# Kernel tuning notes

Hardware: AMD Instinct MI355X
Metric: run time of the kernel (lower is better)

## Reference

```python
import jax, jax.numpy as jnp
import numpy as np

D_MODEL = 1024
D_K = 1024
D_V = 1024
THRESH = 0.9
LN_EPS = 1e-6


def setup_inputs() -> dict:
    key = jax.random.key(0)
    ks = jax.random.split(key, 8)
    B, S = 8, 2048
    scale = 1.0 / np.sqrt(D_MODEL)
    return {
        "q": jax.random.normal(ks[0], (B, S, D_MODEL), dtype=jnp.float32),
        "k": jax.random.normal(ks[1], (B, S, D_MODEL), dtype=jnp.float32),
        "v": jax.random.normal(ks[2], (B, S, D_MODEL), dtype=jnp.float32),
        "Wq": jax.random.normal(ks[3], (D_MODEL, D_K), dtype=jnp.float32) * scale,
        "Wk": jax.random.normal(ks[4], (D_MODEL, D_K), dtype=jnp.float32) * scale,
        "Wv": jax.random.normal(ks[5], (D_MODEL, D_V), dtype=jnp.float32) * scale,
        "Wfc": jax.random.normal(ks[6], (D_V, D_MODEL), dtype=jnp.float32) * (1.0 / np.sqrt(D_V)),
        "ln_gamma": jnp.ones((D_MODEL,), dtype=jnp.float32),
        "ln_beta": jnp.zeros((D_MODEL,), dtype=jnp.float32),
    }


def reference(q, k, v, Wq, Wk, Wv, Wfc, ln_gamma, ln_beta):
    residual = q
    qh = q @ Wq          # [B,S,d_k]
    kh = k @ Wk          # [B,S,d_k]
    vh = v @ Wv          # [B,S,d_v]
    inv_sqrt_dk = jnp.asarray(1.0 / np.sqrt(D_K), dtype=qh.dtype)
    attn = jnp.einsum('bqd,bkd->bqk', qh, kh) * inv_sqrt_dk  # [B,S,S]
    # hard sparsity threshold applied BEFORE softmax (faithful to original)
    attn = jnp.where(attn < THRESH, jnp.asarray(0.0, attn.dtype), attn)
    attn = jax.nn.softmax(attn, axis=-1)
    # dropout is identity in eval mode
    out = jnp.einsum('bqk,bkd->bqd', attn, vh) @ Wfc  # [B,S,d_model]
    out = out + residual
    mean = jnp.mean(out, axis=-1, keepdims=True)
    var = jnp.mean(jnp.square(out - mean), axis=-1, keepdims=True)
    out = (out - mean) * jax.lax.rsqrt(var + LN_EPS) * ln_gamma + ln_beta
    return (out, attn)
```

## Files before the change

kernel.cpp:

```cpp
#include <hip/hip_runtime.h>
#include <hip/hip_bf16.h>
#include <stdint.h>

typedef __attribute__((ext_vector_type(8))) short bf16x8;
typedef __attribute__((ext_vector_type(4))) float f32x4;
typedef __attribute__((ext_vector_type(4))) unsigned short us4;
typedef __attribute__((ext_vector_type(8))) unsigned short us8;

__device__ __forceinline__ unsigned short f2bf(float f) {
  union { float f; unsigned int u; } v; v.f = f;
  unsigned int u = v.u;
  return (unsigned short)((u + 0x7FFFu + ((u >> 16) & 1u)) >> 16);
}
__device__ __forceinline__ float bf2f(unsigned short h) {
  union { unsigned int u; float f; } v; v.u = ((unsigned int)h) << 16;
  return v.f;
}

__device__ __forceinline__ void gload16(const unsigned short* g, unsigned short* l) {
  __builtin_amdgcn_global_load_lds(
      (const __attribute__((address_space(1))) unsigned int*)g,
      (__attribute__((address_space(3))) unsigned int*)l, 16, 0, 0);
}

template <int EPI>
__global__ __launch_bounds__(256, 2)
void gemm_nt(const unsigned short* __restrict__ Ap, const unsigned short* __restrict__ Btp,
             void* __restrict__ Cp, float* __restrict__ extra,
             int M, int N, int K, int nbm,
             long long sA, long long sB, long long sC)
{
  const int tid = threadIdx.x;
  const int lane = tid & 63;
  const int wid = tid >> 6;
  const int wr = wid >> 1, wc = wid & 1;
  const int bb = blockIdx.y;
  const int bm = blockIdx.x % nbm, bn = blockIdx.x / nbm;
  const int row0 = bm * 128, col0 = bn * 128;

  __shared__ unsigned short lsA[128 * 64];
  __shared__ unsigned short lsB[128 * 64];
  __shared__ float srow2[128][2];

  const unsigned short* Ab = Ap + (long long)bb * sA;
  const unsigned short* Bb = Btp + (long long)bb * sB;

  const int srow = wid * 32 + (lane >> 3);
  const int sslot = (lane & 7) ^ (lane >> 3);
  const unsigned short* Asrc = Ab + (long long)(row0 + srow) * K + sslot * 8;
  const unsigned short* Bsrc = Bb + (long long)(col0 + srow) * K + sslot * 8;
  unsigned short* ldsA0 = &lsA[wid * 2048];
  unsigned short* ldsB0 = &lsB[wid * 2048];

  f32x4 acc[4][4];
#pragma unroll
  for (int i = 0; i < 4; ++i)
#pragma unroll
    for (int j = 0; j < 4; ++j) {
      f32x4 z = {0.f, 0.f, 0.f, 0.f};
      acc[i][j] = z;
    }

  for (int k0 = 0; k0 < K; k0 += 64) {
    __syncthreads();
#pragma unroll
    for (int it = 0; it < 4; ++it) {
      gload16(Asrc + (long long)it * 8 * K + k0, ldsA0 + it * 512);
      gload16(Bsrc + (long long)it * 8 * K + k0, ldsB0 + it * 512);
    }
    __syncthreads();
#pragma unroll
    for (int kk = 0; kk < 2; ++kk) {
      int kslot = kk * 4 + (lane >> 4);
      bf16x8 af[4], bfg[4];
#pragma unroll
      for (int mf = 0; mf < 4; ++mf) {
        int rl = wr * 64 + mf * 16 + (lane & 15);
        af[mf] = *(const bf16x8*)&lsA[rl * 64 + ((kslot ^ (rl & 7)) * 8)];
      }
#pragma unroll
      for (int nf = 0; nf < 4; ++nf) {
        int cl = wc * 64 + nf * 16 + (lane & 15);
        bfg[nf] = *(const bf16x8*)&lsB[cl * 64 + ((kslot ^ (cl & 7)) * 8)];
      }
#pragma unroll
      for (int mf = 0; mf < 4; ++mf)
#pragma unroll
        for (int nf = 0; nf < 4; ++nf)
          acc[mf][nf] = __builtin_amdgcn_mfma_f32_16x16x32_bf16(af[mf], bfg[nf], acc[mf][nf], 0, 0, 0);
    }
  }

  if (EPI == 0) {
    unsigned short* C = (unsigned short*)Cp + (long long)bb * sC;
#pragma unroll
    for (int mf = 0; mf < 4; ++mf)
#pragma unroll
      for (int nf = 0; nf < 4; ++nf)
#pragma unroll
        for (int i = 0; i < 4; ++i) {
          int gr = row0 + wr * 64 + mf * 16 + (lane >> 4) * 4 + i;
          int gc = col0 + wc * 64 + nf * 16 + (lane & 15);
          C[(long long)gr * N + gc] = f2bf(acc[mf][nf][i]);
        }
  } else if (EPI == 2) {
    unsigned short* C = (unsigned short*)Cp;
#pragma unroll
    for (int mf = 0; mf < 4; ++mf)
#pragma unroll
      for (int nf = 0; nf < 4; ++nf) {
        int gr = row0 + wr * 64 + mf * 16 + (lane >> 4) * 4;
        int gc = col0 + wc * 64 + nf * 16 + (lane & 15);
        int bb2 = gr >> 11, grb = gr & 2047;
        us4 o;
        o[0] = f2bf(acc[mf][nf][0]); o[1] = f2bf(acc[mf][nf][1]);
        o[2] = f2bf(acc[mf][nf][2]); o[3] = f2bf(acc[mf][nf][3]);
        *(us4*)&C[(long long)bb2 * sC + (long long)gc * 2048 + grb] = o;
      }
  } else if (EPI == 3) {
    unsigned short* C = (unsigned short*)Cp + (long long)bb * sC;
    const float* inv = extra + (long long)bb * 2048;
#pragma unroll
    for (int mf = 0; mf < 4; ++mf)
#pragma unroll
      for (int nf = 0; nf < 4; ++nf)
#pragma unroll
        for (int i = 0; i < 4; ++i) {
          int gr = row0 + wr * 64 + mf * 16 + (lane >> 4) * 4 + i;
          int gc = col0 + wc * 64 + nf * 16 + (lane & 15);
          C[(long long)gr * N + gc] = f2bf(acc[mf][nf][i] * inv[gr]);
        }
  } else {
    unsigned short* C = (unsigned short*)Cp + (long long)bb * sC;
    float rs[4][4];
#pragma unroll
    for (int mf = 0; mf < 4; ++mf)
#pragma unroll
      for (int i = 0; i < 4; ++i) rs[mf][i] = 0.f;
#pragma unroll
    for (int mf = 0; mf < 4; ++mf)
#pragma unroll
      for (int nf = 0; nf < 4; ++nf)
#pragma unroll
        for (int i = 0; i < 4; ++i) {
          int gr = row0 + wr * 64 + mf * 16 + (lane >> 4) * 4 + i;
          int gc = col0 + wc * 64 + nf * 16 + (lane & 15);
          float s = acc[mf][nf][i] * 0.03125f;
          s = (s < 0.9f) ? 0.f : s;
          float e = __expf(s);
          C[(long long)gr * N + gc] = f2bf(e);
          rs[mf][i] += e;
        }
#pragma unroll
    for (int mf = 0; mf < 4; ++mf)
#pragma unroll
      for (int i = 0; i < 4; ++i) {
        float vv = rs[mf][i];
        vv += __shfl_xor(vv, 1); vv += __shfl_xor(vv, 2);
        vv += __shfl_xor(vv, 4); vv += __shfl_xor(vv, 8);
        if ((lane & 15) == 0)
          srow2[wr * 64 + mf * 16 + (lane >> 4) * 4 + i][wc] = vv;
      }
    __syncthreads();
    if (tid < 128) {
      int gr = row0 + tid;
      extra[((long long)bb * M + gr) * 16 + bn] = srow2[tid][0] + srow2[tid][1];
    }
  }
}

__global__ __launch_bounds__(256)
void cvt3(const float* __restrict__ a, const float* __restrict__ b,
          const float* __restrict__ c, unsigned short* __restrict__ oa,
          unsigned short* __restrict__ ob, unsigned short* __restrict__ oc) {
  const long long i = ((long long)blockIdx.x * 256 + threadIdx.x) * 8;
#pragma unroll
  for (int p = 0; p < 3; ++p) {
    const float* src = (p == 0) ? a : (p == 1) ? b : c;
    unsigned short* dst = (p == 0) ? oa : (p == 1) ? ob : oc;
    f32x4 x0 = *(const f32x4*)(src + i);
    f32x4 x1 = *(const f32x4*)(src + i + 4);
    us8 o;
    o[0] = f2bf(x0[0]); o[1] = f2bf(x0[1]); o[2] = f2bf(x0[2]); o[3] = f2bf(x0[3]);
    o[4] = f2bf(x1[0]); o[5] = f2bf(x1[1]); o[6] = f2bf(x1[2]); o[7] = f2bf(x1[3]);
    *(us8*)(dst + i) = o;
  }
}

__global__ __launch_bounds__(256)
void wtrans(const float* __restrict__ W, unsigned short* __restrict__ WT) {
  __shared__ float t[32][33];
  const int bi = blockIdx.x, bj = blockIdx.y;
  const int c = threadIdx.x & 31;
  const int r0 = threadIdx.x >> 5;
#pragma unroll
  for (int j = 0; j < 4; ++j) {
    int r = r0 + j * 8;
    t[r][c] = W[(long long)(bi * 32 + r) * 1024 + bj * 32 + c];
  }
  __syncthreads();
#pragma unroll
  for (int j = 0; j < 4; ++j) {
    int r = r0 + j * 8;
    WT[(long long)(bj * 32 + r) * 1024 + bi * 32 + c] = f2bf(t[c][r]);
  }
}

__global__ __launch_bounds__(256)
void attn_norm(const unsigned short* __restrict__ e, const float* __restrict__ partials,
               float* __restrict__ attn, float* __restrict__ inv_dens) {
  const long long row = blockIdx.x;
  const int tid = threadIdx.x;
  __shared__ float sden;
  if (tid < 64) {
    float v = (tid < 16) ? partials[row * 16 + tid] : 0.f;
    v += __shfl_xor(v, 1); v += __shfl_xor(v, 2);
    v += __shfl_xor(v, 4); v += __shfl_xor(v, 8);
    if (tid == 0) sden = v;
  }
  __syncthreads();
  const float inv = 1.0f / sden;
  if (tid == 0) inv_dens[row] = inv;
  us8 x = *(const us8*)(e + row * 2048 + tid * 8);
  f32x4 y0, y1;
#pragma unroll
  for (int i = 0; i < 4; ++i) { y0[i] = bf2f(x[i]) * inv; y1[i] = bf2f(x[i + 4]) * inv; }
  *(f32x4*)(attn + row * 2048 + tid * 8) = y0;
  *(f32x4*)(attn + row * 2048 + tid * 8 + 4) = y1;
}

__global__ __launch_bounds__(256)
void ln_kernel(const unsigned short* __restrict__ fc, const float* __restrict__ q,
               const float* __restrict__ gamma, const float* __restrict__ beta,
               float* __restrict__ out) {
  const long long row = blockIdx.x;
  const int tid = threadIdx.x;
  __shared__ float sb1[4], sb2[4];
  us4 hv = *(const us4*)(fc + row * 1024 + tid * 4);
  f32x4 qv = *(const f32x4*)(q + row * 1024 + tid * 4);
  float x0 = bf2f(hv[0]) + qv[0];
  float x1 = bf2f(hv[1]) + qv[1];
  float x2 = bf2f(hv[2]) + qv[2];
  float x3 = bf2f(hv[3]) + qv[3];
  float s = x0 + x1 + x2 + x3;
#pragma unroll
  for (int m = 1; m < 64; m <<= 1) s += __shfl_xor(s, m);
  if ((tid & 63) == 0) sb1[tid >> 6] = s;
  __syncthreads();
  const float mean = (sb1[0] + sb1[1] + sb1[2] + sb1[3]) * (1.0f / 1024.0f);
  float d0 = x0 - mean, d1 = x1 - mean, d2 = x2 - mean, d3 = x3 - mean;
  float vs = d0 * d0 + d1 * d1 + d2 * d2 + d3 * d3;
#pragma unroll
  for (int m = 1; m < 64; m <<= 1) vs += __shfl_xor(vs, m);
  if ((tid & 63) == 0) sb2[tid >> 6] = vs;
  __syncthreads();
  const float var = (sb2[0] + sb2[1] + sb2[2] + sb2[3]) * (1.0f / 1024.0f);
  const float r = rsqrtf(var + 1e-6f);
  f32x4 g = *(const f32x4*)(gamma + tid * 4);
  f32x4 bt = *(const f32x4*)(beta + tid * 4);
  f32x4 o;
  o[0] = d0 * r * g[0] + bt[0];
  o[1] = d1 * r * g[1] + bt[1];
  o[2] = d2 * r * g[2] + bt[2];
  o[3] = d3 * r * g[3] + bt[3];
  *(f32x4*)(out + row * 1024 + tid * 4) = o;
}

extern "C" void kernel_launch(void* const* d_in, const int* in_sizes, int n_in,
                              void* d_out, int out_size, void* d_ws, size_t ws_size,
                              hipStream_t stream) {
  const float* q    = (const float*)d_in[0];
  const float* k    = (const float*)d_in[1];
  const float* v    = (const float*)d_in[2];
  const float* Wq   = (const float*)d_in[3];
  const float* Wk   = (const float*)d_in[4];
  const float* Wv   = (const float*)d_in[5];
  const float* Wfc  = (const float*)d_in[6];
  const float* gamma = (const float*)d_in[7];
  const float* beta  = (const float*)d_in[8];

  float* out0 = (float*)d_out;
  float* attn = out0 + (long long)8 * 2048 * 1024;

  char* ao = (char*)attn;
  unsigned short* qb = (unsigned short*)(ao);
  unsigned short* kb = (unsigned short*)(ao + (32ll << 20));
  unsigned short* vb = (unsigned short*)(ao + (64ll << 20));
  unsigned short* qh = (unsigned short*)(ao + (96ll << 20));
  unsigned short* kh = (unsigned short*)(ao);
  unsigned short* vhT     = (unsigned short*)d_out;
  unsigned short* out_mid = (unsigned short*)((char*)d_out + (32ll << 20));

  char* ws = (char*)d_ws;
  unsigned short* WqT  = (unsigned short*)(ws);
  unsigned short* WkT  = (unsigned short*)(ws + (2ll  << 20));
  unsigned short* WvT  = (unsigned short*)(ws + (4ll  << 20));
  unsigned short* WfcT = (unsigned short*)(ws + (6ll  << 20));
  float* partials      = (float*)(ws + (8ll  << 20));
  float* inv_dens      = (float*)(ws + (10ll << 20));
  unsigned short* e    = (unsigned short*)(ws + (11ll << 20));
  unsigned short* fc   = e;

  cvt3<<<dim3(8192), 256, 0, stream>>>(q, k, v, qb, kb, vb);
  wtrans<<<dim3(32, 32), 256, 0, stream>>>(Wq, WqT);
  wtrans<<<dim3(32, 32), 256, 0, stream>>>(Wk, WkT);
  wtrans<<<dim3(32, 32), 256, 0, stream>>>(Wv, WvT);
  wtrans<<<dim3(32, 32), 256, 0, stream>>>(Wfc, WfcT);

  gemm_nt<0><<<dim3(1024, 1), 256, 0, stream>>>(qb, WqT, qh, nullptr,
      16384, 1024, 1024, 128, 0, 0, 0);
  gemm_nt<0><<<dim3(1024, 1), 256, 0, stream>>>(kb, WkT, kh, nullptr,
      16384, 1024, 1024, 128, 0, 0, 0);
  gemm_nt<2><<<dim3(1024, 1), 256, 0, stream>>>(vb, WvT, vhT, nullptr,
      16384, 1024, 1024, 128, 0, 0, 1024ll * 2048);

  gemm_nt<1><<<dim3(256, 8), 256, 0, stream>>>(qh, kh, e, partials,
      2048, 2048, 1024, 16, 2048ll * 1024, 2048ll * 1024, 2048ll * 2048);

  attn_norm<<<dim3(16384), 256, 0, stream>>>(e, partials, attn, inv_dens);

  gemm_nt<3><<<dim3(128, 8), 256, 0, stream>>>(e, vhT, out_mid, inv_dens,
      2048, 1024, 2048, 16, 2048ll * 2048, 1024ll * 2048, 2048ll * 1024);

  gemm_nt<0><<<dim3(1024, 1), 256, 0, stream>>>(out_mid, WfcT, fc, nullptr,
      16384, 1024, 1024, 128, 0, 0, 0);

  ln_kernel<<<dim3(16384), 256, 0, stream>>>(fc, q, gamma, beta, out0);
}
```

Measured before the change: 420.5 us.

## Replace 128x128 GEMM with 256x256 8-wave double-buffered pipelined GEMM

Swaps the 128x128-tile, 4-wave single-buffered GEMM for a 256x256-tile, 8-wave kernel. It double-buffers LDS, prefetches the next K-tile in quarter phases guarded by vmcnt waits, and raises wave priority around the MFMA bursts. The goal is to hide global-load latency behind compute and raise operand reuse per LDS byte. The row-sum partials shrink to 8 per row, so attn_norm changes to match. The cost is 128 KB of LDS per block and fewer blocks, which can leave CUs idle on the smaller batched GEMMs.

Measured after the change: 445.7 us. 6.0% more time.

```diff
diff --git a/kernel.cpp b/kernel.cpp
--- a/kernel.cpp
+++ b/kernel.cpp
@@ -24,149 +24,201 @@
 }
 
 template <int EPI>
-__global__ __launch_bounds__(256, 2)
-void gemm_nt(const unsigned short* __restrict__ Ap, const unsigned short* __restrict__ Btp,
-             void* __restrict__ Cp, float* __restrict__ extra,
-             int M, int N, int K, int nbm,
-             long long sA, long long sB, long long sC)
+__global__ __launch_bounds__(512, 2)
+void gemm8(const unsigned short* __restrict__ Ap, const unsigned short* __restrict__ Btp,
+           void* __restrict__ Cp, float* __restrict__ extra,
+           int M, int N, int K, int nbm, int nbn,
+           long long sA, long long sB, long long sC)
 {
+  __shared__ unsigned short ls[65536];
+  __shared__ float srow[256][4];
+
   const int tid = threadIdx.x;
   const int lane = tid & 63;
   const int wid = tid >> 6;
-  const int wr = wid >> 1, wc = wid & 1;
   const int bb = blockIdx.y;
   const int bm = blockIdx.x % nbm, bn = blockIdx.x / nbm;
-  const int row0 = bm * 128, col0 = bn * 128;
-
-  __shared__ unsigned short lsA[128 * 64];
-  __shared__ unsigned short lsB[128 * 64];
-  __shared__ float srow2[128][2];
+  const int row0 = bm * 256, col0 = bn * 256;
 
   const unsigned short* Ab = Ap + (long long)bb * sA;
   const unsigned short* Bb = Btp + (long long)bb * sB;
 
-  const int srow = wid * 32 + (lane >> 3);
-  const int sslot = (lane & 7) ^ (lane >> 3);
-  const unsigned short* Asrc = Ab + (long long)(row0 + srow) * K + sslot * 8;
-  const unsigned short* Bsrc = Bb + (long long)(col0 + srow) * K + sslot * 8;
-  unsigned short* ldsA0 = &lsA[wid * 2048];
-  unsigned short* ldsB0 = &lsB[wid * 2048];
-
-  f32x4 acc[4][4];
-#pragma unroll
-  for (int i = 0; i < 4; ++i)
-#pragma unroll
-    for (int j = 0; j < 4; ++j) {
-      f32x4 z = {0.f, 0.f, 0.f, 0.f};
-      acc[i][j] = z;
-    }
-
-  for (int k0 = 0; k0 < K; k0 += 64) {
-    __syncthreads();
-#pragma unroll
-    for (int it = 0; it < 4; ++it) {
-      gload16(Asrc + (long long)it * 8 * K + k0, ldsA0 + it * 512);
-      gload16(Bsrc + (long long)it * 8 * K + k0, ldsB0 + it * 512);
-    }
-    __syncthreads();
-#pragma unroll
-    for (int kk = 0; kk < 2; ++kk) {
-      int kslot = kk * 4 + (lane >> 4);
-      bf16x8 af[4], bfg[4];
-#pragma unroll
-      for (int mf = 0; mf < 4; ++mf) {
-        int rl = wr * 64 + mf * 16 + (lane & 15);
-        af[mf] = *(const bf16x8*)&lsA[rl * 64 + ((kslot ^ (rl & 7)) * 8)];
-      }
-#pragma unroll
-      for (int nf = 0; nf < 4; ++nf) {
-        int cl = wc * 64 + nf * 16 + (lane & 15);
-        bfg[nf] = *(const bf16x8*)&lsB[cl * 64 + ((kslot ^ (cl & 7)) * 8)];
-      }
-#pragma unroll
-      for (int mf = 0; mf < 4; ++mf)
-#pragma unroll
-        for (int nf = 0; nf < 4; ++nf)
-          acc[mf][nf] = __builtin_amdgcn_mfma_f32_16x16x32_bf16(af[mf], bfg[nf], acc[mf][nf], 0, 0, 0);
-    }
-  }
-
-  if (EPI == 0) {
+  const int sr = tid >> 3;
+  const int sslot = (tid & 7) ^ (sr & 7);
+  const unsigned short* Asrc = Ab + (long long)(row0 + sr) * K + sslot * 8;
+  const unsigned short* Bsrc = Bb + (long long)(col0 + sr) * K + sslot * 8;
+  unsigned short* lsw = ls + wid * 512;
+
+#define ISSUE_A(HALF, BUFOFF, KOFF) do { \
+    gload16(Asrc + (long long)((HALF) * 128) * K + (KOFF), lsw + (BUFOFF) + (HALF) * 8192); \
+    gload16(Asrc + (long long)((HALF) * 128 + 64) * K + (KOFF), lsw + (BUFOFF) + (HALF) * 8192 + 4096); \
+  } while (0)
+#define ISSUE_B(HALF, BUFOFF, KOFF) do { \
+    gload16(Bsrc + (long long)((HALF) * 128) * K + (KOFF), lsw + (BUFOFF) + (2 + (HALF)) * 8192); \
+    gload16(Bsrc + (long long)((HALF) * 128 + 64) * K + (KOFF), lsw + (BUFOFF) + (2 + (HALF)) * 8192 + 4096); \
+  } while (0)
+
+  const int warow = ((wid >> 2) * 64) + (lane & 15);
+  const int wbcol = ((wid & 3) * 32) + (lane & 15);
+
+  f32x4 acc[2][2][4][2];
+#pragma unroll
+  for (int a = 0; a < 2; ++a)
+#pragma unroll
+    for (int b = 0; b < 2; ++b)
+#pragma unroll
+      for (int m = 0; m < 4; ++m)
+#pragma unroll
+        for (int n = 0; n < 2; ++n) {
+          f32x4 z = {0.f, 0.f, 0.f, 0.f};
+          acc[a][b][m][n] = z;
+        }
+
+#define PHASE(HA, HB) do { \
+    const unsigned short* Ah = ls + cur + (HA) * 8192; \
+    const unsigned short* Bh = ls + cur + (2 + (HB)) * 8192; \
+    _Pragma("unroll") \
+    for (int kk = 0; kk < 2; ++kk) { \
+      const int kslot = kk * 4 + (lane >> 4); \
+      bf16x8 af[4], bfr[2]; \
+      _Pragma("unroll") \
+      for (int mf = 0; mf < 4; ++mf) { \
+        const int rl = warow + mf * 16; \
+        af[mf] = *(const bf16x8*)&Ah[rl * 64 + ((kslot ^ (rl & 7)) * 8)]; \
+      } \
+      _Pragma("unroll") \
+      for (int nf = 0; nf < 2; ++nf) { \
+        const int cl = wbcol + nf * 16; \
+        bfr[nf] = *(const bf16x8*)&Bh[cl * 64 + ((kslot ^ (cl & 7)) * 8)]; \
+      } \
+      __builtin_amdgcn_s_setprio(1); \
+      _Pragma("unroll") \
+      for (int mf = 0; mf < 4; ++mf) \
+        _Pragma("unroll") \
+        for (int nf = 0; nf < 2; ++nf) \
+          acc[HA][HB][mf][nf] = __builtin_amdgcn_mfma_f32_16x16x32_bf16( \
+              af[mf], bfr[nf], acc[HA][HB][mf][nf], 0, 0, 0); \
+      __builtin_amdgcn_s_setprio(0); \
+    } \
+  } while (0)
+
+#define WAITBAR() do { \
+    asm volatile("s_waitcnt vmcnt(4)" ::: "memory"); \
+    __builtin_amdgcn_s_barrier(); \
+    __builtin_amdgcn_sched_barrier(0); \
+  } while (0)
+
+  ISSUE_A(0, 0, 0);
+  ISSUE_B(0, 0, 0);
+  ISSUE_A(1, 0, 0);
+  ISSUE_B(1, 0, 0);
+
+  const int NT = K >> 6;
+  for (int t = 0; t < NT; ++t) {
+    const int cur = (t & 1) << 15;
+    const int nxt = ((t + 1) & 1) << 15;
+    const long long ko = (long long)(t + 1) * 64;
+    const bool pf = (t + 1 < NT);
+    WAITBAR();
+    if (pf) ISSUE_A(0, nxt, ko);
+    PHASE(0, 0);
+    WAITBAR();
+    if (pf) ISSUE_B(0, nxt, ko);
+    PHASE(1, 0);
+    WAITBAR();
+    if (pf) ISSUE_A(1, nxt, ko);
+    PHASE(0, 1);
+    if (pf) ISSUE_B(1, nxt, ko);
+    PHASE(1, 1);
+  }
+
+  if (EPI == 0 || EPI == 3) {
     unsigned short* C = (unsigned short*)Cp + (long long)bb * sC;
-#pragma unroll
-    for (int mf = 0; mf < 4; ++mf)
-#pragma unroll
-      for (int nf = 0; nf < 4; ++nf)
-#pragma unroll
-        for (int i = 0; i < 4; ++i) {
-          int gr = row0 + wr * 64 + mf * 16 + (lane >> 4) * 4 + i;
-          int gc = col0 + wc * 64 + nf * 16 + (lane & 15);
-          C[(long long)gr * N + gc] = f2bf(acc[mf][nf][i]);
-        }
+    const float* inv = (EPI == 3) ? (extra + (long long)bb * 2048) : nullptr;
+#pragma unroll
+    for (int ha = 0; ha < 2; ++ha)
+#pragma unroll
+      for (int hb = 0; hb < 2; ++hb)
+#pragma unroll
+        for (int mf = 0; mf < 4; ++mf)
+#pragma unroll
+          for (int nf = 0; nf < 2; ++nf)
+#pragma unroll
+            for (int i = 0; i < 4; ++i) {
+              int gr = row0 + ha * 128 + (wid >> 2) * 64 + mf * 16 + (lane >> 4) * 4 + i;
+              int gc = col0 + hb * 128 + (wid & 3) * 32 + nf * 16 + (lane & 15);
+              float x = acc[ha][hb][mf][nf][i];
+              if (EPI == 3) x *= inv[gr];
+              C[(long long)gr * N + gc] = f2bf(x);
+            }
   } else if (EPI == 2) {
     unsigned short* C = (unsigned short*)Cp;
 #pragma unroll
-    for (int mf = 0; mf < 4; ++mf)
-#pragma unroll
-      for (int nf = 0; nf < 4; ++nf) {
-        int gr = row0 + wr * 64 + mf * 16 + (lane >> 4) * 4;
-        int gc = col0 + wc * 64 + nf * 16 + (lane & 15);
-        int bb2 = gr >> 11, grb = gr & 2047;
-        us4 o;
-        o[0] = f2bf(acc[mf][nf][0]); o[1] = f2bf(acc[mf][nf][1]);
-        o[2] = f2bf(acc[mf][nf][2]); o[3] = f2bf(acc[mf][nf][3]);
-        *(us4*)&C[(long long)bb2 * sC + (long long)gc * 2048 + grb] = o;
-      }
-  } else if (EPI == 3) {
-    unsigned short* C = (unsigned short*)Cp + (long long)bb * sC;
-    const float* inv = extra + (long long)bb * 2048;
-#pragma unroll
-    for (int mf = 0; mf < 4; ++mf)
-#pragma unroll
-      for (int nf = 0; nf < 4; ++nf)
-#pragma unroll
-        for (int i = 0; i < 4; ++i) {
-          int gr = row0 + wr * 64 + mf * 16 + (lane >> 4) * 4 + i;
-          int gc = col0 + wc * 64 + nf * 16 + (lane & 15);
-          C[(long long)gr * N + gc] = f2bf(acc[mf][nf][i] * inv[gr]);
-        }
+    for (int ha = 0; ha < 2; ++ha)
+#pragma unroll
+      for (int hb = 0; hb < 2; ++hb)
+#pragma unroll
+        for (int mf = 0; mf < 4; ++mf)
+#pragma unroll
+          for (int nf = 0; nf < 2; ++nf) {
+            int gr = row0 + ha * 128 + (wid >> 2) * 64 + mf * 16 + (lane >> 4) * 4;
+            int gc = col0 + hb * 128 + (wid & 3) * 32 + nf * 16 + (lane & 15);
+            int bb2 = gr >> 11, grb = gr & 2047;
+            us4 o;
+            o[0] = f2bf(acc[ha][hb][mf][nf][0]); o[1] = f2bf(acc[ha][hb][mf][nf][1]);
+            o[2] = f2bf(acc[ha][hb][mf][nf][2]); o[3] = f2bf(acc[ha][hb][mf][nf][3]);
+            *(us4*)&C[(long long)bb2 * sC + (long long)gc * 2048 + grb] = o;
+          }
   } else {
     unsigned short* C = (unsigned short*)Cp + (long long)bb * sC;
-    float rs[4][4];
-#pragma unroll
-    for (int mf = 0; mf < 4; ++mf)
-#pragma unroll
-      for (int i = 0; i < 4; ++i) rs[mf][i] = 0.f;
-#pragma unroll
-    for (int mf = 0; mf < 4; ++mf)
-#pragma unroll
-      for (int nf = 0; nf < 4; ++nf)
+    float rs[2][4][4];
+#pragma unroll
+    for (int ha = 0; ha < 2; ++ha)
+#pragma unroll
+      for (int mf = 0; mf < 4; ++mf)
+#pragma unroll
+        for (int i = 0; i < 4; ++i) rs[ha][mf][i] = 0.f;
+#pragma unroll
+    for (int ha = 0; ha < 2; ++ha)
+#pragma unroll
+      for (int hb = 0; hb < 2; ++hb)
+#pragma unroll
+        for (int mf = 0; mf < 4; ++mf)
+#pragma unroll
+          for (int nf = 0; nf < 2; ++nf)
+#pragma unroll
+            for (int i = 0; i < 4; ++i) {
+              int gr = row0 + ha * 128 + (wid >> 2) * 64 + mf * 16 + (lane >> 4) * 4 + i;
+              int gc = col0 + hb * 128 + (wid & 3) * 32 + nf * 16 + (lane & 15);
+              float s = acc[ha][hb][mf][nf][i] * 0.03125f;
+              s = (s < 0.9f) ? 0.f : s;
+              float e = __expf(s);
+              C[(long long)gr * N + gc] = f2bf(e);
+              rs[ha][mf][i] += e;
+            }
+#pragma unroll
+    for (int ha = 0; ha < 2; ++ha)
+#pragma unroll
+      for (int mf = 0; mf < 4; ++mf)
 #pragma unroll
         for (int i = 0; i < 4; ++i) {
-          int gr = row0 + wr * 64 + mf * 16 + (lane >> 4) * 4 + i;
-          int gc = col0 + wc * 64 + nf * 16 + (lane & 15);
-          float s = acc[mf][nf][i] * 0.03125f;
-          s = (s < 0.9f) ? 0.f : s;
-          float e = __expf(s);
-          C[(long long)gr * N + gc] = f2bf(e);
-          rs[mf][i] += e;
+          float vv = rs[ha][mf][i];
+          vv += __shfl_xor(vv, 1); vv += __shfl_xor(vv, 2);
+          vv += __shfl_xor(vv, 4); vv += __shfl_xor(vv, 8);
+          if ((lane & 15) == 0)
+            srow[ha * 128 + (wid >> 2) * 64 + mf * 16 + (lane >> 4) * 4 + i][wid & 3] = vv;
         }
-#pragma unroll
-    for (int mf = 0; mf < 4; ++mf)
-#pragma unroll
-      for (int i = 0; i < 4; ++i) {
-        float vv = rs[mf][i];
-        vv += __shfl_xor(vv, 1); vv += __shfl_xor(vv, 2);
-        vv += __shfl_xor(vv, 4); vv += __shfl_xor(vv, 8);
-        if ((lane & 15) == 0)
-          srow2[wr * 64 + mf * 16 + (lane >> 4) * 4 + i][wc] = vv;
-      }
     __syncthreads();
-    if (tid < 128) {
+    if (tid < 256) {
       int gr = row0 + tid;
-      extra[((long long)bb * M + gr) * 16 + bn] = srow2[tid][0] + srow2[tid][1];
+      extra[((long long)bb * M + gr) * nbn + bn] =
+          srow[tid][0] + srow[tid][1] + srow[tid][2] + srow[tid][3];
     }
   }
+#undef PHASE
+#undef WAITBAR
+#undef ISSUE_A
+#undef ISSUE_B
 }
 
 __global__ __launch_bounds__(256)
@@ -213,9 +265,8 @@
   const int tid = threadIdx.x;
   __shared__ float sden;
   if (tid < 64) {
-    float v = (tid < 16) ? partials[row * 16 + tid] : 0.f;
-    v += __shfl_xor(v, 1); v += __shfl_xor(v, 2);
-    v += __shfl_xor(v, 4); v += __shfl_xor(v, 8);
+    float v = (tid < 8) ? partials[row * 8 + tid] : 0.f;
+    v += __shfl_xor(v, 1); v += __shfl_xor(v, 2); v += __shfl_xor(v, 4);
     if (tid == 0) sden = v;
   }
   __syncthreads();
@@ -307,23 +358,23 @@
   wtrans<<<dim3(32, 32), 256, 0, stream>>>(Wv, WvT);
   wtrans<<<dim3(32, 32), 256, 0, stream>>>(Wfc, WfcT);
 
-  gemm_nt<0><<<dim3(1024, 1), 256, 0, stream>>>(qb, WqT, qh, nullptr,
-      16384, 1024, 1024, 128, 0, 0, 0);
-  gemm_nt<0><<<dim3(1024, 1), 256, 0, stream>>>(kb, WkT, kh, nullptr,
-      16384, 1024, 1024, 128, 0, 0, 0);
-  gemm_nt<2><<<dim3(1024, 1), 256, 0, stream>>>(vb, WvT, vhT, nullptr,
-      16384, 1024, 1024, 128, 0, 0, 1024ll * 2048);
-
-  gemm_nt<1><<<dim3(256, 8), 256, 0, stream>>>(qh, kh, e, partials,
-      2048, 2048, 1024, 16, 2048ll * 1024, 2048ll * 1024, 2048ll * 2048);
+  gemm8<0><<<dim3(256, 1), 512, 0, stream>>>(qb, WqT, qh, nullptr,
+      16384, 1024, 1024, 64, 4, 0, 0, 0);
+  gemm8<0><<<dim3(256, 1), 512, 0, stream>>>(kb, WkT, kh, nullptr,
+      16384, 1024, 1024, 64, 4, 0, 0, 0);
+  gemm8<2><<<dim3(256, 1), 512, 0, stream>>>(vb, WvT, vhT, nullptr,
+      16384, 1024, 1024, 64, 4, 0, 0, 1024ll * 2048);
+
+  gemm8<1><<<dim3(64, 8), 512, 0, stream>>>(qh, kh, e, partials,
+      2048, 2048, 1024, 8, 8, 2048ll * 1024, 2048ll * 1024, 2048ll * 2048);
 
   attn_norm<<<dim3(16384), 256, 0, stream>>>(e, partials, attn, inv_dens);
 
-  gemm_nt<3><<<dim3(128, 8), 256, 0, stream>>>(e, vhT, out_mid, inv_dens,
-      2048, 1024, 2048, 16, 2048ll * 2048, 1024ll * 2048, 2048ll * 1024);
-
-  gemm_nt<0><<<dim3(1024, 1), 256, 0, stream>>>(out_mid, WfcT, fc, nullptr,
-      16384, 1024, 1024, 128, 0, 0, 0);
+  gemm8<3><<<dim3(32, 8), 512, 0, stream>>>(e, vhT, out_mid, inv_dens,
+      2048, 1024, 2048, 8, 4, 2048ll * 2048, 1024ll * 2048, 2048ll * 1024);
+
+  gemm8<0><<<dim3(256, 1), 512, 0, stream>>>(out_mid, WfcT, fc, nullptr,
+      16384, 1024, 1024, 64, 4, 0, 0, 0);
 
   ln_kernel<<<dim3(16384), 256, 0, stream>>>(fc, q, gamma, beta, out0);
 }
```

## Replace GEMM with 256x256-tile triple-buffered pipelined kernel using 8 waves

Applied to the files above, without the earlier changes.

Replaces the 128x128, 256-thread GEMM with a 256x256-tile, 512-thread kernel that keeps three BK=32 LDS buffers and prefetches two K-steps ahead, using explicit vmcnt waits and a single barrier per step. It also raises MFMA priority around the compute block and reduces per-tile row-sum partials from 16 to 8, updating attn_norm to match. The aim is to overlap global loads with MFMA and raise arithmetic intensity per LDS byte. In exchange, register pressure is much higher (8x4 accumulators), occupancy drops to one block per CU, and the grids shrink to 256 blocks, which may underfill the 256 CUs for some launches.

New measurement: 446.2 us. 1.06x slower.

```diff
diff --git a/kernel.cpp b/kernel.cpp
--- a/kernel.cpp
+++ b/kernel.cpp
@@ -24,127 +24,131 @@
 }
 
 template <int EPI>
-__global__ __launch_bounds__(256, 2)
-void gemm_nt(const unsigned short* __restrict__ Ap, const unsigned short* __restrict__ Btp,
-             void* __restrict__ Cp, float* __restrict__ extra,
-             int M, int N, int K, int nbm,
-             long long sA, long long sB, long long sC)
+__global__ __launch_bounds__(512, 1)
+void gemm9(const unsigned short* __restrict__ Ap, const unsigned short* __restrict__ Btp,
+           void* __restrict__ Cp, float* __restrict__ extra,
+           int M, int N, int K, int nbm, int nbn,
+           long long sA, long long sB, long long sC)
 {
+  __shared__ unsigned short ls[3 * 16384];
+  __shared__ float srow[256][4];
+
   const int tid = threadIdx.x;
   const int lane = tid & 63;
   const int wid = tid >> 6;
-  const int wr = wid >> 1, wc = wid & 1;
   const int bb = blockIdx.y;
   const int bm = blockIdx.x % nbm, bn = blockIdx.x / nbm;
-  const int row0 = bm * 128, col0 = bn * 128;
-
-  __shared__ unsigned short lsA[128 * 64];
-  __shared__ unsigned short lsB[128 * 64];
-  __shared__ float srow2[128][2];
+  const int row0 = bm * 256, col0 = bn * 256;
 
   const unsigned short* Ab = Ap + (long long)bb * sA;
   const unsigned short* Bb = Btp + (long long)bb * sB;
 
-  const int srow = wid * 32 + (lane >> 3);
-  const int sslot = (lane & 7) ^ (lane >> 3);
-  const unsigned short* Asrc = Ab + (long long)(row0 + srow) * K + sslot * 8;
-  const unsigned short* Bsrc = Bb + (long long)(col0 + srow) * K + sslot * 8;
-  unsigned short* ldsA0 = &lsA[wid * 2048];
-  unsigned short* ldsB0 = &lsB[wid * 2048];
-
-  f32x4 acc[4][4];
-#pragma unroll
-  for (int i = 0; i < 4; ++i)
-#pragma unroll
-    for (int j = 0; j < 4; ++j) {
+  const int stgrow = wid * 32 + (lane >> 2);
+  const int sslot = (lane & 3) ^ ((lane >> 2) & 3);
+  const unsigned short* Asrc = Ab + (long long)(row0 + stgrow) * K + sslot * 8;
+  const unsigned short* Bsrc = Bb + (long long)(col0 + stgrow) * K + sslot * 8;
+
+  const int warow = (wid >> 2) * 128 + (lane & 15);
+  const int wbcol = (wid & 3) * 64 + (lane & 15);
+  const int rslot = ((lane >> 4) ^ (lane & 3)) * 8;
+
+#define ISSUE(KT, CB) do { \
+    unsigned short* _la = ls + (CB) * 16384 + wid * 1024; \
+    unsigned short* _lb = _la + 8192; \
+    const long long _ko = (long long)(KT) * 32; \
+    gload16(Asrc + _ko, _la); \
+    gload16(Asrc + 16ll * K + _ko, _la + 512); \
+    gload16(Bsrc + _ko, _lb); \
+    gload16(Bsrc + 16ll * K + _ko, _lb + 512); \
+  } while (0)
+
+  f32x4 acc[8][4];
+#pragma unroll
+  for (int m = 0; m < 8; ++m)
+#pragma unroll
+    for (int n = 0; n < 4; ++n) {
       f32x4 z = {0.f, 0.f, 0.f, 0.f};
-      acc[i][j] = z;
+      acc[m][n] = z;
     }
 
-  for (int k0 = 0; k0 < K; k0 += 64) {
-    __syncthreads();
-#pragma unroll
-    for (int it = 0; it < 4; ++it) {
-      gload16(Asrc + (long long)it * 8 * K + k0, ldsA0 + it * 512);
-      gload16(Bsrc + (long long)it * 8 * K + k0, ldsB0 + it * 512);
+  const int NT = K >> 5;
+  ISSUE(0, 0);
+  ISSUE(1, 1);
+
+  int c0 = 0, c1 = 1, c2 = 2;
+  for (int t = 0; t < NT; ++t) {
+    if (t + 1 < NT) asm volatile("s_waitcnt vmcnt(4)" ::: "memory");
+    else            asm volatile("s_waitcnt vmcnt(0)" ::: "memory");
+    __builtin_amdgcn_s_barrier();
+    __builtin_amdgcn_sched_barrier(0);
+    if (t + 2 < NT) ISSUE(t + 2, c2);
+    {
+      const unsigned short* _A = ls + c0 * 16384;
+      const unsigned short* _B = _A + 8192;
+      bf16x8 af[8], bfr[4];
+#pragma unroll
+      for (int mf = 0; mf < 8; ++mf)
+        af[mf] = *(const bf16x8*)&_A[(warow + mf * 16) * 32 + rslot];
+#pragma unroll
+      for (int nf = 0; nf < 4; ++nf)
+        bfr[nf] = *(const bf16x8*)&_B[(wbcol + nf * 16) * 32 + rslot];
+      __builtin_amdgcn_s_setprio(1);
+#pragma unroll
+      for (int mf = 0; mf < 8; ++mf)
+#pragma unroll
+        for (int nf = 0; nf < 4; ++nf)
+          acc[mf][nf] = __builtin_amdgcn_mfma_f32_16x16x32_bf16(
+              af[mf], bfr[nf], acc[mf][nf], 0, 0, 0);
+      __builtin_amdgcn_s_setprio(0);
     }
-    __syncthreads();
-#pragma unroll
-    for (int kk = 0; kk < 2; ++kk) {
-      int kslot = kk * 4 + (lane >> 4);
-      bf16x8 af[4], bfg[4];
-#pragma unroll
-      for (int mf = 0; mf < 4; ++mf) {
-        int rl = wr * 64 + mf * 16 + (lane & 15);
-        af[mf] = *(const bf16x8*)&lsA[rl * 64 + ((kslot ^ (rl & 7)) * 8)];
-      }
-#pragma unroll
-      for (int nf = 0; nf < 4; ++nf) {
-        int cl = wc * 64 + nf * 16 + (lane & 15);
-        bfg[nf] = *(const bf16x8*)&lsB[cl * 64 + ((kslot ^ (cl & 7)) * 8)];
-      }
-#pragma unroll
-      for (int mf = 0; mf < 4; ++mf)
-#pragma unroll
-        for (int nf = 0; nf < 4; ++nf)
-          acc[mf][nf] = __builtin_amdgcn_mfma_f32_16x16x32_bf16(af[mf], bfg[nf], acc[mf][nf], 0, 0, 0);
-    }
-  }
-
-  if (EPI == 0) {
+    int tmp = c0; c0 = c1; c1 = c2; c2 = tmp;
+  }
+#undef ISSUE
+
+  if (EPI == 0 || EPI == 3) {
     unsigned short* C = (unsigned short*)Cp + (long long)bb * sC;
-#pragma unroll
-    for (int mf = 0; mf < 4; ++mf)
+    const float* inv = (EPI == 3) ? (extra + (long long)bb * 2048) : nullptr;
+#pragma unroll
+    for (int mf = 0; mf < 8; ++mf)
 #pragma unroll
       for (int nf = 0; nf < 4; ++nf)
 #pragma unroll
         for (int i = 0; i < 4; ++i) {
-          int gr = row0 + wr * 64 + mf * 16 + (lane >> 4) * 4 + i;
-          int gc = col0 + wc * 64 + nf * 16 + (lane & 15);
-          C[(long long)gr * N + gc] = f2bf(acc[mf][nf][i]);
+          int gr = row0 + (wid >> 2) * 128 + mf * 16 + (lane >> 4) * 4 + i;
+          int gc = col0 + (wid & 3) * 64 + nf * 16 + (lane & 15);
+          float x = acc[mf][nf][i];
+          if (EPI == 3) x *= inv[gr];
+          C[(long long)gr * N + gc] = f2bf(x);
         }
   } else if (EPI == 2) {
     unsigned short* C = (unsigned short*)Cp;
 #pragma unroll
-    for (int mf = 0; mf < 4; ++mf)
+    for (int mf = 0; mf < 8; ++mf)
 #pragma unroll
       for (int nf = 0; nf < 4; ++nf) {
-        int gr = row0 + wr * 64 + mf * 16 + (lane >> 4) * 4;
-        int gc = col0 + wc * 64 + nf * 16 + (lane & 15);
+        int gr = row0 + (wid >> 2) * 128 + mf * 16 + (lane >> 4) * 4;
+        int gc = col0 + (wid & 3) * 64 + nf * 16 + (lane & 15);
         int bb2 = gr >> 11, grb = gr & 2047;
         us4 o;
         o[0] = f2bf(acc[mf][nf][0]); o[1] = f2bf(acc[mf][nf][1]);
         o[2] = f2bf(acc[mf][nf][2]); o[3] = f2bf(acc[mf][nf][3]);
         *(us4*)&C[(long long)bb2 * sC + (long long)gc * 2048 + grb] = o;
       }
-  } else if (EPI == 3) {
-    unsigned short* C = (unsigned short*)Cp + (long long)bb * sC;
-    const float* inv = extra + (long long)bb * 2048;
-#pragma unroll
-    for (int mf = 0; mf < 4; ++mf)
-#pragma unroll
-      for (int nf = 0; nf < 4; ++nf)
-#pragma unroll
-        for (int i = 0; i < 4; ++i) {
-          int gr = row0 + wr * 64 + mf * 16 + (lane >> 4) * 4 + i;
-          int gc = col0 + wc * 64 + nf * 16 + (lane & 15);
-          C[(long long)gr * N + gc] = f2bf(acc[mf][nf][i] * inv[gr]);
-        }
   } else {
     unsigned short* C = (unsigned short*)Cp + (long long)bb * sC;
-    float rs[4][4];
-#pragma unroll
-    for (int mf = 0; mf < 4; ++mf)
+    float rs[8][4];
+#pragma unroll
+    for (int mf = 0; mf < 8; ++mf)
 #pragma unroll
       for (int i = 0; i < 4; ++i) rs[mf][i] = 0.f;
 #pragma unroll
-    for (int mf = 0; mf < 4; ++mf)
+    for (int mf = 0; mf < 8; ++mf)
 #pragma unroll
       for (int nf = 0; nf < 4; ++nf)
 #pragma unroll
         for (int i = 0; i < 4; ++i) {
-          int gr = row0 + wr * 64 + mf * 16 + (lane >> 4) * 4 + i;
-          int gc = col0 + wc * 64 + nf * 16 + (lane & 15);
+          int gr = row0 + (wid >> 2) * 128 + mf * 16 + (lane >> 4) * 4 + i;
+          int gc = col0 + (wid & 3) * 64 + nf * 16 + (lane & 15);
           float s = acc[mf][nf][i] * 0.03125f;
           s = (s < 0.9f) ? 0.f : s;
           float e = __expf(s);
@@ -152,19 +156,20 @@
           rs[mf][i] += e;
         }
 #pragma unroll
-    for (int mf = 0; mf < 4; ++mf)
+    for (int mf = 0; mf < 8; ++mf)
 #pragma unroll
       for (int i = 0; i < 4; ++i) {
         float vv = rs[mf][i];
         vv += __shfl_xor(vv, 1); vv += __shfl_xor(vv, 2);
         vv += __shfl_xor(vv, 4); vv += __shfl_xor(vv, 8);
         if ((lane & 15) == 0)
-          srow2[wr * 64 + mf * 16 + (lane >> 4) * 4 + i][wc] = vv;
+          srow[(wid >> 2) * 128 + mf * 16 + (lane >> 4) * 4 + i][wid & 3] = vv;
       }
     __syncthreads();
-    if (tid < 128) {
+    if (tid < 256) {
       int gr = row0 + tid;
-      extra[((long long)bb * M + gr) * 16 + bn] = srow2[tid][0] + srow2[tid][1];
+      extra[((long long)bb * M + gr) * nbn + bn] =
+          srow[tid][0] + srow[tid][1] + srow[tid][2] + srow[tid][3];
     }
   }
 }
@@ -213,9 +218,8 @@
   const int tid = threadIdx.x;
   __shared__ float sden;
   if (tid < 64) {
-    float v = (tid < 16) ? partials[row * 16 + tid] : 0.f;
-    v += __shfl_xor(v, 1); v += __shfl_xor(v, 2);
-    v += __shfl_xor(v, 4); v += __shfl_xor(v, 8);
+    float v = (tid < 8) ? partials[row * 8 + tid] : 0.f;
+    v += __shfl_xor(v, 1); v += __shfl_xor(v, 2); v += __shfl_xor(v, 4);
     if (tid == 0) sden = v;
   }
   __syncthreads();
@@ -307,23 +311,23 @@
   wtrans<<<dim3(32, 32), 256, 0, stream>>>(Wv, WvT);
   wtrans<<<dim3(32, 32), 256, 0, stream>>>(Wfc, WfcT);
 
-  gemm_nt<0><<<dim3(1024, 1), 256, 0, stream>>>(qb, WqT, qh, nullptr,
-      16384, 1024, 1024, 128, 0, 0, 0);
-  gemm_nt<0><<<dim3(1024, 1), 256, 0, stream>>>(kb, WkT, kh, nullptr,
-      16384, 1024, 1024, 128, 0, 0, 0);
-  gemm_nt<2><<<dim3(1024, 1), 256, 0, stream>>>(vb, WvT, vhT, nullptr,
-      16384, 1024, 1024, 128, 0, 0, 1024ll * 2048);
-
-  gemm_nt<1><<<dim3(256, 8), 256, 0, stream>>>(qh, kh, e, partials,
-      2048, 2048, 1024, 16, 2048ll * 1024, 2048ll * 1024, 2048ll * 2048);
+  gemm9<0><<<dim3(256, 1), 512, 0, stream>>>(qb, WqT, qh, nullptr,
+      16384, 1024, 1024, 64, 4, 0, 0, 0);
+  gemm9<0><<<dim3(256, 1), 512, 0, stream>>>(kb, WkT, kh, nullptr,
+      16384, 1024, 1024, 64, 4, 0, 0, 0);
+  gemm9<2><<<dim3(256, 1), 512, 0, stream>>>(vb, WvT, vhT, nullptr,
+      16384, 1024, 1024, 64, 4, 0, 0, 1024ll * 2048);
+
+  gemm9<1><<<dim3(64, 8), 512, 0, stream>>>(qh, kh, e, partials,
+      2048, 2048, 1024, 8, 8, 2048ll * 1024, 2048ll * 1024, 2048ll * 2048);
 
   attn_norm<<<dim3(16384), 256, 0, stream>>>(e, partials, attn, inv_dens);
 
-  gemm_nt<3><<<dim3(128, 8), 256, 0, stream>>>(e, vhT, out_mid, inv_dens,
-      2048, 1024, 2048, 16, 2048ll * 2048, 1024ll * 2048, 2048ll * 1024);
-
-  gemm_nt<0><<<dim3(1024, 1), 256, 0, stream>>>(out_mid, WfcT, fc, nullptr,
-      16384, 1024, 1024, 128, 0, 0, 0);
+  gemm9<3><<<dim3(32, 8), 512, 0, stream>>>(e, vhT, out_mid, inv_dens,
+      2048, 1024, 2048, 8, 4, 2048ll * 2048, 1024ll * 2048, 2048ll * 1024);
+
+  gemm9<0><<<dim3(256, 1), 512, 0, stream>>>(out_mid, WfcT, fc, nullptr,
+      16384, 1024, 1024, 64, 4, 0, 0, 0);
 
   ln_kernel<<<dim3(16384), 256, 0, stream>>>(fc, q, gamma, beta, out0);
 }
```
